# Optimization experiments

Hardware: AMD Instinct MI355X
Metric: run time of the kernel (lower is better)

## Reference

```python
import jax, jax.numpy as jnp
import numpy as np

RES_H, RES_W = 64, 64
INV_SMOOTHNESS = 0.1
OFFSET = 0.5
LOSS_WEIGHT = 1.0


def bilinear_sample(mask, xs, ys):
    # mask: [IH, IW]; xs: [Wo]; ys: [Ho] in pixel coords -> [Ho, Wo]
    IH, IW = mask.shape
    x0 = jnp.floor(xs); y0 = jnp.floor(ys)
    wx = xs - x0; wy = ys - y0
    x0i = jnp.clip(x0.astype(jnp.int32), 0, IW - 1)
    x1i = jnp.clip(x0i + 1, 0, IW - 1)
    y0i = jnp.clip(y0.astype(jnp.int32), 0, IH - 1)
    y1i = jnp.clip(y0i + 1, 0, IH - 1)
    g = lambda yi, xi: mask[yi[:, None], xi[None, :]]
    return ((1 - wy)[:, None] * ((1 - wx)[None, :] * g(y0i, x0i) + wx[None, :] * g(y0i, x1i))
            + wy[:, None] * ((1 - wx)[None, :] * g(y1i, x0i) + wx[None, :] * g(y1i, x1i)))


def crop_and_resize(masks, boxes, Ho, Wo):
    # masks: [N, IH, IW]; boxes: [N, 4] xyxy -> binarized [N, Ho, Wo]
    def one(mask, box):
        x1, y1, x2, y2 = box[0], box[1], box[2], box[3]
        xs = x1 + (x2 - x1) * (jnp.arange(Wo, dtype=masks.dtype) + 0.5) / Wo - 0.5
        ys = y1 + (y2 - y1) * (jnp.arange(Ho, dtype=masks.dtype) + 0.5) / Ho - 0.5
        return bilinear_sample(mask, xs, ys)
    out = jax.vmap(one)(masks, boxes)
    return (out >= 0.5).astype(masks.dtype)


def rasterize_mask(verts, H, W, inv_s):
    # Soft polygon rasterization, MODE_MASK: sigmoid(sign * min_sq_dist * inv_s).
    # verts: [N, V, 2] (x, y) in pixel coords of the HxW grid.
    N, V, _ = verts.shape
    xs = jnp.arange(W, dtype=verts.dtype)
    ys = jnp.arange(H, dtype=verts.dtype)
    px = jnp.tile(xs, H)       # [P] with P = H*W
    py = jnp.repeat(ys, W)     # [P]
    p = jnp.stack([px, py], -1)  # [P, 2]
    a = verts                          # [N, V, 2]
    b = jnp.roll(verts, -1, axis=1)    # next vertex (closed polygon)
    ab = b - a                         # [N, V, 2]
    denom = jnp.sum(ab * ab, -1)       # [N, V]
    pa = p[None, :, None, :] - a[:, None, :, :]            # [N, P, V, 2]
    t = jnp.clip(jnp.einsum('npvc,nvc->npv', pa, ab) / (denom[:, None, :] + 1e-12), 0.0, 1.0)
    diff = pa - t[..., None] * ab[:, None, :, :]
    d2 = jnp.sum(diff * diff, -1)      # [N, P, V] squared point-to-segment dist
    d2min = jnp.min(d2, -1)            # [N, P]
    # even-odd crossing test for inside/outside sign
    ay = a[..., 1][:, None, :]; by = b[..., 1][:, None, :]     # [N, 1, V]
    pyb = py[None, :, None]
    cond = (ay > pyb) != (by > pyb)                             # [N, P, V]
    dy = ab[..., 1][:, None, :]
    safe_dy = jnp.where(dy == 0, 1.0, dy)
    xint = a[..., 0][:, None, :] + (pyb - ay) * ab[..., 0][:, None, :] / safe_dy
    crossings = jnp.sum((cond & (px[None, :, None] < xint)).astype(jnp.int32), -1)  # [N, P]
    sign = jnp.where(crossings % 2 == 1, 1.0, -1.0)
    return jax.nn.sigmoid(sign * d2min * inv_s).reshape(N, H, W)


def dice_loss(inp, tgt):
    n = inp.shape[0]
    smooth = 1.0
    iflat = inp.reshape(n, -1)
    tflat = tgt.reshape(n, -1)
    inter = jnp.sum(iflat * tflat, -1)
    losses = 1.0 - (2.0 * inter + smooth) / (jnp.sum(iflat, -1) + jnp.sum(tflat, -1) + smooth)
    return jnp.sum(losses) / n


def setup_inputs() -> dict:
    key = jax.random.key(0)
    k1, k2, k3, k4, k5, k6 = jax.random.split(key, 6)
    N, V, IMG = 128, 128, 512
    # star-shaped polygons (realistic contours) in image coords
    ctr = jax.random.uniform(k1, (N, 1, 2)) * (IMG * 0.6) + IMG * 0.2
    ang = jnp.linspace(0.0, 2.0 * jnp.pi, V, endpoint=False)
    rad = 20.0 + jax.random.uniform(k2, (N, V)) * 60.0
    preds = ctr + jnp.stack([rad * jnp.cos(ang), rad * jnp.sin(ang)], -1)  # [N, V, 2]
    # gt boxes xyxy
    x1y1 = jax.random.uniform(k3, (N, 2)) * (IMG * 0.3)
    wh = 50.0 + jax.random.uniform(k4, (N, 2)) * (IMG * 0.4)
    targets_bboxes = jnp.concatenate([x1y1, x1y1 + wh], -1)  # [N, 4]
    # gt full-image masks: random disks
    cb = jax.random.uniform(k5, (N, 2)) * IMG
    r = 30.0 + jax.random.uniform(k6, (N,)) * 100.0
    yy = jnp.arange(IMG, dtype=jnp.float32)[None, :, None]
    xx = jnp.arange(IMG, dtype=jnp.float32)[None, None, :]
    targets_masks = (((xx - cb[:, 0, None, None]) ** 2 + (yy - cb[:, 1, None, None]) ** 2)
                     < (r[:, None, None] ** 2)).astype(jnp.float32)  # [N, IMG, IMG]
    return {"preds": preds, "targets_masks": targets_masks, "targets_bboxes": targets_bboxes}


def reference(preds, targets_masks, targets_bboxes):
    # union bboxes of predicted polygon extent and gt bbox
    pmin = jnp.min(preds, axis=1)
    pmax = jnp.max(preds, axis=1)
    ub = jnp.concatenate([jnp.minimum(pmin, targets_bboxes[:, :2]),
                          jnp.maximum(pmax, targets_bboxes[:, 2:4])], -1)  # [N, 4]
    # crop + resize + binarize gt masks at the union boxes
    tgt = crop_and_resize(targets_masks, ub, RES_H, RES_W)  # [N, 64, 64]
    # normalize polygons into the (detached) union box
    ubd = jax.lax.stop_gradient(ub)
    normed = (preds - ubd[:, None, :2]) / (ubd[:, None, 2:4] - ubd[:, None, :2])
    verts = normed * float(RES_W) - OFFSET
    pred_masks = rasterize_mask(verts, RES_H, RES_W, INV_SMOOTHNESS)  # [N, 64, 64]
    pred_masks = jnp.clip(pred_masks, 1e-5, 0.99999)
    return dice_loss(pred_masks, tgt) * LOSS_WEIGHT
```

## Files before the change

### kernel.cpp

```cpp
#include <hip/hip_runtime.h>
#include <hip/hip_bf16.h>

#define NMASK 128
#define NV    128
#define IMG   512
#define RES   64
#define PB    8
#define PPB   (RES*RES/PB)
#define BT    256


__device__ __forceinline__ int clampi(int v, int lo, int hi) {
    return v < lo ? lo : (v > hi ? hi : v);
}

__device__ __forceinline__ int detect_bf16(const void* preds) {
    const __hip_bfloat16* pb = (const __hip_bfloat16*)preds;
    int lane = threadIdx.x & 63;
    float v = __bfloat162float(pb[2 * lane]);
    bool ok = (v >= 1.0f) && (v <= 600.0f);
    unsigned long long m = __ballot(ok);
    return (m == 0xFFFFFFFFFFFFFFFFULL) ? 1 : 0;
}

__device__ __forceinline__ float loadf(const void* p, long idx, int isb) {
    if (isb) return __bfloat162float(((const __hip_bfloat16*)p)[idx]);
    return ((const float*)p)[idx];
}

__global__ void __launch_bounds__(64) ub_kernel(
    const void* __restrict__ preds,
    const void* __restrict__ bboxes,
    float* __restrict__ ub,
    float* __restrict__ acc)
{
    int n = blockIdx.x, t = threadIdx.x;
    int isb = detect_bf16(preds);
    long base = (long)n * NV * 2;
    float x0 = loadf(preds, base + 2*t,          isb);
    float y0 = loadf(preds, base + 2*t + 1,      isb);
    float x1 = loadf(preds, base + 2*(t+64),     isb);
    float y1 = loadf(preds, base + 2*(t+64) + 1, isb);
    float mnx = fminf(x0, x1), mxx = fmaxf(x0, x1);
    float mny = fminf(y0, y1), mxy = fmaxf(y0, y1);
    for (int off = 32; off >= 1; off >>= 1) {
        mnx = fminf(mnx, __shfl_xor(mnx, off));
        mxx = fmaxf(mxx, __shfl_xor(mxx, off));
        mny = fminf(mny, __shfl_xor(mny, off));
        mxy = fmaxf(mxy, __shfl_xor(mxy, off));
    }
    if (t == 0) {
        float bx1 = loadf(bboxes, n*4 + 0, isb);
        float by1 = loadf(bboxes, n*4 + 1, isb);
        float bx2 = loadf(bboxes, n*4 + 2, isb);
        float by2 = loadf(bboxes, n*4 + 3, isb);
        ub[n*4+0] = fminf(mnx, bx1);
        ub[n*4+1] = fminf(mny, by1);
        ub[n*4+2] = fmaxf(mxx, bx2);
        ub[n*4+3] = fmaxf(mxy, by2);
        acc[n*3+0] = 0.0f;
        acc[n*3+1] = 0.0f;
        acc[n*3+2] = 0.0f;
    }
}

__global__ void __launch_bounds__(BT) MaskRasterizationLoss_2705829396671_kernel(
    const void* __restrict__ preds,
    const void* __restrict__ masks,
    const float* __restrict__ ub,
    float* __restrict__ acc)
{
    int n    = blockIdx.x >> 3;
    int part = blockIdx.x & 7;
    int t    = threadIdx.x;

    int isb = detect_bf16(preds);

    __shared__ __align__(16) float ed[NV][8];

    float ux1 = ub[n*4+0], uy1 = ub[n*4+1], ux2 = ub[n*4+2], uy2 = ub[n*4+3];
    float sx = (float)RES / (ux2 - ux1);
    float sy = (float)RES / (uy2 - uy1);

    if (t < NV) {
        float vx = loadf(preds, ((long)n*NV + t)*2 + 0, isb);
        float vy = loadf(preds, ((long)n*NV + t)*2 + 1, isb);
        ed[t][0] = (vx - ux1) * sx - 0.5f;
        ed[t][1] = (vy - uy1) * sy - 0.5f;
    }
    __syncthreads();
    if (t < NV) {
        int tn = (t + 1) & (NV - 1);
        float ax = ed[t][0],  ay = ed[t][1];
        float bx = ed[tn][0], by = ed[tn][1];
        float abx = bx - ax, aby = by - ay;
        ed[t][2] = abx;
        ed[t][3] = aby;
        ed[t][4] = 1.0f / (abx*abx + aby*aby + 1e-12f);
        ed[t][5] = abx / ((aby == 0.0f) ? 1.0f : aby);
        ed[t][6] = by;
        ed[t][7] = 0.0f;
    }
    __syncthreads();

    int p0 = part * PPB + t;
    int p1 = p0 + BT;
    float px0 = (float)(p0 & (RES-1)), py0 = (float)(p0 >> 6);
    float px1 = (float)(p1 & (RES-1)), py1 = (float)(p1 >> 6);

    float d2min0 = 1e30f, d2min1 = 1e30f;
    int cross0 = 0, cross1 = 0;

    #pragma unroll 4
    for (int v = 0; v < NV; ++v) {
        const float4* e4 = reinterpret_cast<const float4*>(&ed[v][0]);
        float4 e0 = e4[0];
        float4 e1 = e4[1];

        {
            float pax = px0 - e0.x, pay = py0 - e0.y;
            float tt = (pax*e0.z + pay*e0.w) * e1.x;
            tt = fminf(fmaxf(tt, 0.0f), 1.0f);
            float dx = pax - tt*e0.z, dy = pay - tt*e0.w;
            float d2 = dx*dx + dy*dy;
            d2min0 = fminf(d2min0, d2);
            bool c = (e0.y > py0) != (e1.z > py0);
            float xint = e0.x + pay * e1.y;
            cross0 ^= (c && (px0 < xint)) ? 1 : 0;
        }
        {
            float pax = px1 - e0.x, pay = py1 - e0.y;
            float tt = (pax*e0.z + pay*e0.w) * e1.x;
            tt = fminf(fmaxf(tt, 0.0f), 1.0f);
            float dx = pax - tt*e0.z, dy = pay - tt*e0.w;
            float d2 = dx*dx + dy*dy;
            d2min1 = fminf(d2min1, d2);
            bool c = (e0.y > py1) != (e1.z > py1);
            float xint = e0.x + pay * e1.y;
            cross1 ^= (c && (px1 < xint)) ? 1 : 0;
        }
    }

    long mbase = (long)n * IMG * IMG;
    float s_pred = 0.0f, s_tgt = 0.0f, s_int = 0.0f;

    #pragma unroll
    for (int k = 0; k < 2; ++k) {
        float px = k ? px1 : px0;
        float py = k ? py1 : py0;
        float d2min = k ? d2min1 : d2min0;
        int   cross = k ? cross1 : cross0;

        float sign = (cross & 1) ? 1.0f : -1.0f;
        float z = sign * d2min * 0.1f;
        float sgm = 1.0f / (1.0f + __expf(-z));
        sgm = fminf(fmaxf(sgm, 1e-5f), 0.99999f);

        float xs = ux1 + (ux2 - ux1) * (px + 0.5f) * (1.0f/(float)RES) - 0.5f;
        float ys = uy1 + (uy2 - uy1) * (py + 0.5f) * (1.0f/(float)RES) - 0.5f;
        float fx = floorf(xs), fy = floorf(ys);
        float wx = xs - fx,   wy = ys - fy;
        int x0i = clampi((int)fx, 0, IMG-1);
        int x1i = clampi(x0i + 1, 0, IMG-1);
        int y0i = clampi((int)fy, 0, IMG-1);
        int y1i = clampi(y0i + 1, 0, IMG-1);
        float g00 = loadf(masks, mbase + (long)y0i*IMG + x0i, isb);
        float g01 = loadf(masks, mbase + (long)y0i*IMG + x1i, isb);
        float g10 = loadf(masks, mbase + (long)y1i*IMG + x0i, isb);
        float g11 = loadf(masks, mbase + (long)y1i*IMG + x1i, isb);
        float bil = (1.0f-wy) * ((1.0f-wx)*g00 + wx*g01)
                  +        wy * ((1.0f-wx)*g10 + wx*g11);
        float tgt = (bil >= 0.5f) ? 1.0f : 0.0f;

        s_pred += sgm;
        s_tgt  += tgt;
        s_int  += sgm * tgt;
    }

    for (int off = 32; off >= 1; off >>= 1) {
        s_pred += __shfl_xor(s_pred, off);
        s_tgt  += __shfl_xor(s_tgt,  off);
        s_int  += __shfl_xor(s_int,  off);
    }
    __shared__ float red[3][4];
    int wave = t >> 6;
    if ((t & 63) == 0) { red[0][wave] = s_pred; red[1][wave] = s_tgt; red[2][wave] = s_int; }
    __syncthreads();
    if (t == 0) {
        float a0 = red[0][0] + red[0][1] + red[0][2] + red[0][3];
        float a1 = red[1][0] + red[1][1] + red[1][2] + red[1][3];
        float a2 = red[2][0] + red[2][1] + red[2][2] + red[2][3];
        atomicAdd(&acc[n*3+0], a0);
        atomicAdd(&acc[n*3+1], a1);
        atomicAdd(&acc[n*3+2], a2);
    }
}

__global__ void __launch_bounds__(128) finalize_kernel(
    const float* __restrict__ acc, void* __restrict__ out)
{
    int t = threadIdx.x;
    float sp = acc[t*3+0], st = acc[t*3+1], si = acc[t*3+2];
    float loss = 1.0f - (2.0f*si + 1.0f) / (sp + st + 1.0f);
    for (int off = 32; off >= 1; off >>= 1)
        loss += __shfl_xor(loss, off);
    __shared__ float tmp[2];
    if ((t & 63) == 0) tmp[t >> 6] = loss;
    __syncthreads();
    if (t == 0) {
        float L = (tmp[0] + tmp[1]) * (1.0f/128.0f);
        unsigned int fb = __float_as_uint(L);
        unsigned int r  = (fb + 0x7FFFu + ((fb >> 16) & 1u)) >> 16;
        ((unsigned int*)out)[0] = (r << 16) | r;
    }
}

extern "C" void kernel_launch(void* const* d_in, const int* in_sizes, int n_in,
                              void* d_out, int out_size, void* d_ws, size_t ws_size,
                              hipStream_t stream) {
    const void* preds  = d_in[0];
    const void* masks  = d_in[1];
    const void* bboxes = d_in[2];

    float* ws  = (float*)d_ws;
    float* ub  = ws;
    float* acc = ws + 512;

    ub_kernel<<<NMASK, 64, 0, stream>>>(preds, bboxes, ub, acc);
    MaskRasterizationLoss_2705829396671_kernel<<<NMASK * PB, BT, 0, stream>>>(preds, masks, ub, acc);
    finalize_kernel<<<1, 128, 0, stream>>>(acc, d_out);
}
```

Measured before the change: 197.1 us.

## Precompute edges in setup kernel, fold finalize into last block, 4 pixels/thread

Edge precomputation (normalized vertices, edge vectors, inverse lengths, slopes) moves into a setup kernel that writes them to workspace, so the main kernel only copies them into shared memory. The finalize kernel is removed: a last-block-done atomic counter lets the final block compute the dice loss, saving one launch. Each thread now handles 4 adjacent pixels in a row, which lets per-edge row terms (crossing condition, intersection x, y products) and the bilinear y-coordinates be shared, with FMAs used throughout. Blocks per mask drop from 8 to 4, so the grid is half as large and each thread does more work, which may reduce parallelism.

```diff
diff --git a/kernel.cpp b/kernel.cpp
--- a/kernel.cpp
+++ b/kernel.cpp
@@ -5,10 +5,15 @@
 #define NV    128
 #define IMG   512
 #define RES   64
-#define PB    8
-#define PPB   (RES*RES/PB)
+#define PB    4
+#define NBLK  (NMASK*PB)
 #define BT    256
 
+#define EDGES_OFF 0
+#define UB_OFF    131072
+#define ACC_OFF   131584
+#define CNT_OFF   131968
+#define FLAG_OFF  131969
 
 __device__ __forceinline__ int clampi(int v, int lo, int hi) {
     return v < lo ? lo : (v > hi ? hi : v);
@@ -28,153 +33,155 @@
     return ((const float*)p)[idx];
 }
 
-__global__ void __launch_bounds__(64) ub_kernel(
+__global__ void __launch_bounds__(128) setup_kernel(
     const void* __restrict__ preds,
     const void* __restrict__ bboxes,
-    float* __restrict__ ub,
-    float* __restrict__ acc)
+    float* __restrict__ ws)
 {
     int n = blockIdx.x, t = threadIdx.x;
     int isb = detect_bf16(preds);
-    long base = (long)n * NV * 2;
-    float x0 = loadf(preds, base + 2*t,          isb);
-    float y0 = loadf(preds, base + 2*t + 1,      isb);
-    float x1 = loadf(preds, base + 2*(t+64),     isb);
-    float y1 = loadf(preds, base + 2*(t+64) + 1, isb);
-    float mnx = fminf(x0, x1), mxx = fmaxf(x0, x1);
-    float mny = fminf(y0, y1), mxy = fmaxf(y0, y1);
+
+    float vx = loadf(preds, ((long)n*NV + t)*2 + 0, isb);
+    float vy = loadf(preds, ((long)n*NV + t)*2 + 1, isb);
+
+    float mnx = vx, mxx = vx, mny = vy, mxy = vy;
     for (int off = 32; off >= 1; off >>= 1) {
         mnx = fminf(mnx, __shfl_xor(mnx, off));
         mxx = fmaxf(mxx, __shfl_xor(mxx, off));
         mny = fminf(mny, __shfl_xor(mny, off));
         mxy = fmaxf(mxy, __shfl_xor(mxy, off));
     }
-    if (t == 0) {
-        float bx1 = loadf(bboxes, n*4 + 0, isb);
-        float by1 = loadf(bboxes, n*4 + 1, isb);
-        float bx2 = loadf(bboxes, n*4 + 2, isb);
-        float by2 = loadf(bboxes, n*4 + 3, isb);
-        ub[n*4+0] = fminf(mnx, bx1);
-        ub[n*4+1] = fminf(mny, by1);
-        ub[n*4+2] = fmaxf(mxx, bx2);
-        ub[n*4+3] = fmaxf(mxy, by2);
-        acc[n*3+0] = 0.0f;
-        acc[n*3+1] = 0.0f;
-        acc[n*3+2] = 0.0f;
-    }
-}
-
-__global__ void __launch_bounds__(BT) MaskRasterizationLoss_2705829396671_kernel(
-    const void* __restrict__ preds,
-    const void* __restrict__ masks,
-    const float* __restrict__ ub,
-    float* __restrict__ acc)
-{
-    int n    = blockIdx.x >> 3;
-    int part = blockIdx.x & 7;
-    int t    = threadIdx.x;
-
-    int isb = detect_bf16(preds);
-
-    __shared__ __align__(16) float ed[NV][8];
-
-    float ux1 = ub[n*4+0], uy1 = ub[n*4+1], ux2 = ub[n*4+2], uy2 = ub[n*4+3];
+    __shared__ float r[2][4];
+    int w = t >> 6;
+    if ((t & 63) == 0) { r[w][0]=mnx; r[w][1]=mxx; r[w][2]=mny; r[w][3]=mxy; }
+    __syncthreads();
+    mnx = fminf(r[0][0], r[1][0]);
+    mxx = fmaxf(r[0][1], r[1][1]);
+    mny = fminf(r[0][2], r[1][2]);
+    mxy = fmaxf(r[0][3], r[1][3]);
+
+    float bx1 = loadf(bboxes, n*4 + 0, isb);
+    float by1 = loadf(bboxes, n*4 + 1, isb);
+    float bx2 = loadf(bboxes, n*4 + 2, isb);
+    float by2 = loadf(bboxes, n*4 + 3, isb);
+    float ux1 = fminf(mnx, bx1), uy1 = fminf(mny, by1);
+    float ux2 = fmaxf(mxx, bx2), uy2 = fmaxf(mxy, by2);
     float sx = (float)RES / (ux2 - ux1);
     float sy = (float)RES / (uy2 - uy1);
 
-    if (t < NV) {
-        float vx = loadf(preds, ((long)n*NV + t)*2 + 0, isb);
-        float vy = loadf(preds, ((long)n*NV + t)*2 + 1, isb);
-        ed[t][0] = (vx - ux1) * sx - 0.5f;
-        ed[t][1] = (vy - uy1) * sy - 0.5f;
-    }
-    __syncthreads();
-    if (t < NV) {
-        int tn = (t + 1) & (NV - 1);
-        float ax = ed[t][0],  ay = ed[t][1];
-        float bx = ed[tn][0], by = ed[tn][1];
-        float abx = bx - ax, aby = by - ay;
-        ed[t][2] = abx;
-        ed[t][3] = aby;
-        ed[t][4] = 1.0f / (abx*abx + aby*aby + 1e-12f);
-        ed[t][5] = abx / ((aby == 0.0f) ? 1.0f : aby);
-        ed[t][6] = by;
-        ed[t][7] = 0.0f;
-    }
-    __syncthreads();
-
-    int p0 = part * PPB + t;
-    int p1 = p0 + BT;
-    float px0 = (float)(p0 & (RES-1)), py0 = (float)(p0 >> 6);
-    float px1 = (float)(p1 & (RES-1)), py1 = (float)(p1 >> 6);
-
-    float d2min0 = 1e30f, d2min1 = 1e30f;
-    int cross0 = 0, cross1 = 0;
+    __shared__ float2 vn[NV];
+    vn[t] = make_float2((vx - ux1)*sx - 0.5f, (vy - uy1)*sy - 0.5f);
+    __syncthreads();
+
+    float2 a = vn[t];
+    float2 b = vn[(t + 1) & (NV - 1)];
+    float abx = b.x - a.x, aby = b.y - a.y;
+    float inv = 1.0f / (abx*abx + aby*aby + 1e-12f);
+    float slope = abx / ((aby == 0.0f) ? 1.0f : aby);
+
+    float4* eg = (float4*)(ws + EDGES_OFF + (size_t)n * NV * 8);
+    eg[2*t]   = make_float4(a.x, a.y, abx, aby);
+    eg[2*t+1] = make_float4(inv, slope, b.y, 0.0f);
+
+    if (t == 0) {
+        ws[UB_OFF + n*4 + 0] = ux1;
+        ws[UB_OFF + n*4 + 1] = uy1;
+        ws[UB_OFF + n*4 + 2] = ux2;
+        ws[UB_OFF + n*4 + 3] = uy2;
+        ws[ACC_OFF + n*3 + 0] = 0.0f;
+        ws[ACC_OFF + n*3 + 1] = 0.0f;
+        ws[ACC_OFF + n*3 + 2] = 0.0f;
+        if (n == 0) {
+            ((int*)ws)[CNT_OFF]  = 0;
+            ((int*)ws)[FLAG_OFF] = isb;
+        }
+    }
+}
+
+__global__ void __launch_bounds__(BT) MaskRasterizationLoss_2705829396671_kernel(
+    const void* __restrict__ masks,
+    float* __restrict__ ws,
+    void* __restrict__ out)
+{
+    int n    = blockIdx.x >> 2;
+    int part = blockIdx.x & 3;
+    int t    = threadIdx.x;
+
+    __shared__ __align__(16) float4 eds[NV*2];
+    __shared__ float red[3][4];
+    __shared__ int   s_last;
+    __shared__ float fin[2];
+
+    const float4* eg = (const float4*)(ws + EDGES_OFF + (size_t)n * NV * 8);
+    eds[t] = eg[t];
+
+    float ux1 = ws[UB_OFF + n*4 + 0], uy1 = ws[UB_OFF + n*4 + 1];
+    float ux2 = ws[UB_OFF + n*4 + 2], uy2 = ws[UB_OFF + n*4 + 3];
+    int isb = ((const int*)ws)[FLAG_OFF];
+    float* acc = ws + ACC_OFF;
+    __syncthreads();
+
+    int p0 = part * 1024 + t * 4;
+    float py  = (float)(p0 >> 6);
+    float pxb = (float)(p0 & 63);
+
+    float d2m[4] = {1e30f, 1e30f, 1e30f, 1e30f};
+    int   cr[4]  = {0, 0, 0, 0};
 
     #pragma unroll 4
     for (int v = 0; v < NV; ++v) {
-        const float4* e4 = reinterpret_cast<const float4*>(&ed[v][0]);
-        float4 e0 = e4[0];
-        float4 e1 = e4[1];
-
-        {
-            float pax = px0 - e0.x, pay = py0 - e0.y;
-            float tt = (pax*e0.z + pay*e0.w) * e1.x;
+        float4 e0 = eds[2*v];
+        float4 e1 = eds[2*v+1];
+        float pay  = py - e0.y;
+        float q    = pay * e0.w;
+        bool  cnd  = (e0.y > py) != (e1.z > py);
+        float xint = fmaf(pay, e1.y, e0.x);
+        #pragma unroll
+        for (int k = 0; k < 4; ++k) {
+            float px  = pxb + (float)k;
+            float pax = px - e0.x;
+            float tt  = fmaf(pax, e0.z, q) * e1.x;
             tt = fminf(fmaxf(tt, 0.0f), 1.0f);
-            float dx = pax - tt*e0.z, dy = pay - tt*e0.w;
-            float d2 = dx*dx + dy*dy;
-            d2min0 = fminf(d2min0, d2);
-            bool c = (e0.y > py0) != (e1.z > py0);
-            float xint = e0.x + pay * e1.y;
-            cross0 ^= (c && (px0 < xint)) ? 1 : 0;
-        }
-        {
-            float pax = px1 - e0.x, pay = py1 - e0.y;
-            float tt = (pax*e0.z + pay*e0.w) * e1.x;
-            tt = fminf(fmaxf(tt, 0.0f), 1.0f);
-            float dx = pax - tt*e0.z, dy = pay - tt*e0.w;
-            float d2 = dx*dx + dy*dy;
-            d2min1 = fminf(d2min1, d2);
-            bool c = (e0.y > py1) != (e1.z > py1);
-            float xint = e0.x + pay * e1.y;
-            cross1 ^= (c && (px1 < xint)) ? 1 : 0;
+            float dx  = fmaf(-tt, e0.z, pax);
+            float dyv = fmaf(-tt, e0.w, pay);
+            float d2  = fmaf(dx, dx, dyv*dyv);
+            d2m[k] = fminf(d2m[k], d2);
+            cr[k] ^= (cnd && (px < xint)) ? 1 : 0;
         }
     }
 
     long mbase = (long)n * IMG * IMG;
+    float invW = (ux2 - ux1) * (1.0f/(float)RES);
+    float invH = (uy2 - uy1) * (1.0f/(float)RES);
+    float ys = fmaf(py + 0.5f, invH, uy1) - 0.5f;
+    float fy = floorf(ys), wy = ys - fy;
+    int y0i = clampi((int)fy, 0, IMG-1);
+    int y1i = clampi(y0i + 1, 0, IMG-1);
+
     float s_pred = 0.0f, s_tgt = 0.0f, s_int = 0.0f;
-
     #pragma unroll
-    for (int k = 0; k < 2; ++k) {
-        float px = k ? px1 : px0;
-        float py = k ? py1 : py0;
-        float d2min = k ? d2min1 : d2min0;
-        int   cross = k ? cross1 : cross0;
-
-        float sign = (cross & 1) ? 1.0f : -1.0f;
-        float z = sign * d2min * 0.1f;
-        float sgm = 1.0f / (1.0f + __expf(-z));
-        sgm = fminf(fmaxf(sgm, 1e-5f), 0.99999f);
-
-        float xs = ux1 + (ux2 - ux1) * (px + 0.5f) * (1.0f/(float)RES) - 0.5f;
-        float ys = uy1 + (uy2 - uy1) * (py + 0.5f) * (1.0f/(float)RES) - 0.5f;
-        float fx = floorf(xs), fy = floorf(ys);
-        float wx = xs - fx,   wy = ys - fy;
+    for (int k = 0; k < 4; ++k) {
+        float px = pxb + (float)k;
+        float sgn = (cr[k] & 1) ? 1.0f : -1.0f;
+        float z = sgn * d2m[k] * 0.1f;
+        float sg = 1.0f / (1.0f + __expf(-z));
+        sg = fminf(fmaxf(sg, 1e-5f), 0.99999f);
+
+        float xs = fmaf(px + 0.5f, invW, ux1) - 0.5f;
+        float fx = floorf(xs), wx = xs - fx;
         int x0i = clampi((int)fx, 0, IMG-1);
         int x1i = clampi(x0i + 1, 0, IMG-1);
-        int y0i = clampi((int)fy, 0, IMG-1);
-        int y1i = clampi(y0i + 1, 0, IMG-1);
         float g00 = loadf(masks, mbase + (long)y0i*IMG + x0i, isb);
         float g01 = loadf(masks, mbase + (long)y0i*IMG + x1i, isb);
         float g10 = loadf(masks, mbase + (long)y1i*IMG + x0i, isb);
         float g11 = loadf(masks, mbase + (long)y1i*IMG + x1i, isb);
         float bil = (1.0f-wy) * ((1.0f-wx)*g00 + wx*g01)
                   +        wy * ((1.0f-wx)*g10 + wx*g11);
-        float tgt = (bil >= 0.5f) ? 1.0f : 0.0f;
-
-        s_pred += sgm;
-        s_tgt  += tgt;
-        s_int  += sgm * tgt;
+        float tg = (bil >= 0.5f) ? 1.0f : 0.0f;
+
+        s_pred += sg;
+        s_tgt  += tg;
+        s_int  += sg * tg;
     }
 
     for (int off = 32; off >= 1; off >>= 1) {
@@ -182,36 +189,39 @@
         s_tgt  += __shfl_xor(s_tgt,  off);
         s_int  += __shfl_xor(s_int,  off);
     }
-    __shared__ float red[3][4];
     int wave = t >> 6;
-    if ((t & 63) == 0) { red[0][wave] = s_pred; red[1][wave] = s_tgt; red[2][wave] = s_int; }
+    if ((t & 63) == 0) { red[0][wave]=s_pred; red[1][wave]=s_tgt; red[2][wave]=s_int; }
     __syncthreads();
     if (t == 0) {
-        float a0 = red[0][0] + red[0][1] + red[0][2] + red[0][3];
-        float a1 = red[1][0] + red[1][1] + red[1][2] + red[1][3];
-        float a2 = red[2][0] + red[2][1] + red[2][2] + red[2][3];
-        atomicAdd(&acc[n*3+0], a0);
-        atomicAdd(&acc[n*3+1], a1);
-        atomicAdd(&acc[n*3+2], a2);
-    }
-}
-
-__global__ void __launch_bounds__(128) finalize_kernel(
-    const float* __restrict__ acc, void* __restrict__ out)
-{
-    int t = threadIdx.x;
-    float sp = acc[t*3+0], st = acc[t*3+1], si = acc[t*3+2];
-    float loss = 1.0f - (2.0f*si + 1.0f) / (sp + st + 1.0f);
-    for (int off = 32; off >= 1; off >>= 1)
-        loss += __shfl_xor(loss, off);
-    __shared__ float tmp[2];
-    if ((t & 63) == 0) tmp[t >> 6] = loss;
-    __syncthreads();
-    if (t == 0) {
-        float L = (tmp[0] + tmp[1]) * (1.0f/128.0f);
-        unsigned int fb = __float_as_uint(L);
-        unsigned int r  = (fb + 0x7FFFu + ((fb >> 16) & 1u)) >> 16;
-        ((unsigned int*)out)[0] = (r << 16) | r;
+        atomicAdd(&acc[n*3+0], red[0][0]+red[0][1]+red[0][2]+red[0][3]);
+        atomicAdd(&acc[n*3+1], red[1][0]+red[1][1]+red[1][2]+red[1][3]);
+        atomicAdd(&acc[n*3+2], red[2][0]+red[2][1]+red[2][2]+red[2][3]);
+        __threadfence();
+        int old = atomicAdd((int*)ws + CNT_OFF, 1);
+        s_last = (old == NBLK - 1) ? 1 : 0;
+    }
+    __syncthreads();
+
+    if (s_last) {
+        __threadfence();
+        float loss = 0.0f;
+        if (t < NMASK) {
+            float sp = atomicAdd(&acc[t*3+0], 0.0f);
+            float st = atomicAdd(&acc[t*3+1], 0.0f);
+            float si = atomicAdd(&acc[t*3+2], 0.0f);
+            loss = 1.0f - (2.0f*si + 1.0f) / (sp + st + 1.0f);
+        }
+        for (int off = 32; off >= 1; off >>= 1)
+            loss += __shfl_xor(loss, off);
+        if (t == 0)  fin[0] = loss;
+        if (t == 64) fin[1] = loss;
+        __syncthreads();
+        if (t == 0) {
+            float L = (fin[0] + fin[1]) * (1.0f/(float)NMASK);
+            unsigned int fb = __float_as_uint(L);
+            unsigned int r  = (fb + 0x7FFFu + ((fb >> 16) & 1u)) >> 16;
+            ((unsigned int*)out)[0] = (r << 16) | r;
+        }
     }
 }
 
@@ -221,12 +231,8 @@
     const void* preds  = d_in[0];
     const void* masks  = d_in[1];
     const void* bboxes = d_in[2];
-
-    float* ws  = (float*)d_ws;
-    float* ub  = ws;
-    float* acc = ws + 512;
-
-    ub_kernel<<<NMASK, 64, 0, stream>>>(preds, bboxes, ub, acc);
-    MaskRasterizationLoss_2705829396671_kernel<<<NMASK * PB, BT, 0, stream>>>(preds, masks, ub, acc);
-    finalize_kernel<<<1, 128, 0, stream>>>(acc, d_out);
-}
+    float* ws = (float*)d_ws;
+
+    setup_kernel<<<NMASK, 128, 0, stream>>>(preds, bboxes, ws);
+    MaskRasterizationLoss_2705829396671_kernel<<<NBLK, BT, 0, stream>>>(masks, ws, d_out);
+}
```

After: 211.2 us. 1.07x slower.
